# Kernel tuning notes

Measured on AMD Instinct MI355X. Metric: run time of the kernel, lower is better.

Reference implementation:

```python
import jax, jax.numpy as jnp
import numpy as np

N_CLASSES = 10
NBD_PAD = 1
EPS = 1e-5  # nn.LayerNorm default eps


def _neighbor_states(state, n):
    # state: [B, n_classes, H, W]; replicates F.unfold(kernel=2n+1, padding=n)
    # then drops the center tap. Kernel positions enumerated row-major, matching
    # unfold's (C, K2) channel ordering after the view in the torch code.
    B, C, H, W = state.shape
    k = 2 * n + 1
    center = (k * k) // 2
    padded = jnp.pad(state, ((0, 0), (0, 0), (n, n), (n, n)))
    shifts = []
    for idx in range(k * k):
        if idx == center:
            continue
        ki, kj = divmod(idx, k)
        shifts.append(padded[:, :, ki:ki + H, kj:kj + W])
    nb = jnp.stack(shifts, axis=2)  # [B, C, K2-1, H, W]
    return nb.reshape(B, C * (k * k - 1), H, W)


def setup_inputs() -> dict:
    key = jax.random.key(0)
    ks = jax.random.split(key, 7)
    B, C, H, W = 64, 32, 128, 128
    NN_HID, PERC = 128, 112
    x = jax.random.normal(ks[0], (B, C, H, W), dtype=jnp.float32)
    w1 = jax.random.normal(ks[1], (NN_HID, PERC), dtype=jnp.float32) * (1.0 / np.sqrt(PERC))
    b1 = jax.random.normal(ks[2], (NN_HID,), dtype=jnp.float32) * 0.02
    w2 = jax.random.normal(ks[3], (C, NN_HID), dtype=jnp.float32) * (1.0 / np.sqrt(NN_HID))
    b2 = jax.random.normal(ks[4], (C,), dtype=jnp.float32) * 0.02
    gamma = jnp.ones((C,), dtype=jnp.float32) + 0.1 * jax.random.normal(ks[5], (C,), dtype=jnp.float32)
    beta = 0.1 * jax.random.normal(ks[6], (C,), dtype=jnp.float32)
    return {"x": x, "w1": w1, "b1": b1, "w2": w2, "b2": b2, "gamma": gamma, "beta": beta}


def reference(x, w1, b1, w2, b2, gamma, beta):
    # perceive: [B, in_ch + n_classes*(K2-1), H, W]
    nb = _neighbor_states(x[:, :N_CLASSES], NBD_PAD)
    perc = jnp.concatenate([x, nb], axis=1)
    # 1x1 conv MLP (fire_rate == 1.0 -> no update mask)
    h = jax.nn.relu(jnp.einsum('bchw,oc->bohw', perc, w1) + b1[None, :, None, None])
    dx = jnp.einsum('bchw,oc->bohw', h, w2) + b2[None, :, None, None]
    new_state = x + dx
    # clean_slate_if_white: zero hidden channels where argmax class == 0 (no_grad mask)
    pred = jnp.argmax(new_state[:, :N_CLASSES], axis=1)  # [B,H,W]
    inv = jax.lax.stop_gradient((pred != 0).astype(new_state.dtype))[:, None]  # [B,1,H,W]
    new_state = jnp.concatenate(
        [new_state[:, :N_CLASSES], new_state[:, N_CLASSES:] * inv], axis=1)
    # LayerNorm over channel dim (torch permutes to NHWC, norms last dim, permutes back)
    mu = jnp.mean(new_state, axis=1, keepdims=True)
    var = jnp.var(new_state, axis=1, keepdims=True)
    xn = (new_state - mu) * jax.lax.rsqrt(var + EPS)
    return xn * gamma[None, :, None, None] + beta[None, :, None, None]
```

## Files before the change

kernel.cpp:

```cpp
#include <hip/hip_runtime.h>

typedef unsigned short U16;
typedef unsigned int U32;
typedef __bf16 bf16;
typedef bf16 bf16x8 __attribute__((ext_vector_type(8)));
typedef U16  u16x8  __attribute__((ext_vector_type(8)));
typedef float f32x4 __attribute__((ext_vector_type(4)));

__device__ __forceinline__ void split3(float a, U16& o1, U16& o2, U16& o3) {
    U32 ua = __float_as_uint(a);
    float a1 = __uint_as_float(ua & 0xFFFF0000u);
    float r1 = a - a1;
    U32 u2 = __float_as_uint(r1);
    float a2 = __uint_as_float(u2 & 0xFFFF0000u);
    float r2 = r1 - a2;
    o1 = (U16)(ua >> 16);
    o2 = (U16)(u2 >> 16);
    o3 = (U16)(__float_as_uint(r2) >> 16);
}

__device__ __forceinline__ void split3x8(const float v[8], bf16x8& A1, bf16x8& A2, bf16x8& A3) {
    u16x8 e1, e2, e3;
    #pragma unroll
    for (int j = 0; j < 8; ++j) { U16 a, b, c; split3(v[j], a, b, c); e1[j] = a; e2[j] = b; e3[j] = c; }
    A1 = __builtin_bit_cast(bf16x8, e1);
    A2 = __builtin_bit_cast(bf16x8, e2);
    A3 = __builtin_bit_cast(bf16x8, e3);
}

__global__ __launch_bounds__(256)
void prep_kernel(const float* __restrict__ w1g, const float* __restrict__ w2g,
                 U16* __restrict__ w1L, U16* __restrict__ w2L)
{
    int tid = blockIdx.x * 256 + threadIdx.x;
    if (tid < 2048) {
        int n = tid >> 4, k0 = (tid & 15) << 3;
        float v[8];
        #pragma unroll
        for (int j = 0; j < 8; ++j) { int k = k0 + j; v[j] = (k < 112) ? w1g[n * 112 + k] : 0.0f; }
        bf16x8 L1, L2, L3; split3x8(v, L1, L2, L3);
        *(bf16x8*)(w1L + 0 * 16384 + n * 128 + k0) = L1;
        *(bf16x8*)(w1L + 1 * 16384 + n * 128 + k0) = L2;
        *(bf16x8*)(w1L + 2 * 16384 + n * 128 + k0) = L3;
    }
    if (tid < 512) {
        int n = tid >> 4, k0 = (tid & 15) << 3;
        float v[8];
        #pragma unroll
        for (int j = 0; j < 8; ++j) v[j] = w2g[n * 128 + k0 + j];
        bf16x8 L1, L2, L3; split3x8(v, L1, L2, L3);
        *(bf16x8*)(w2L + 0 * 4096 + n * 128 + k0) = L1;
        *(bf16x8*)(w2L + 1 * 4096 + n * 128 + k0) = L2;
        *(bf16x8*)(w2L + 2 * 4096 + n * 128 + k0) = L3;
    }
}

__device__ __forceinline__ void tap_load(const float* __restrict__ xg, int b, int irow,
                                         int jbase, int j, float v[8])
{
    int tpx = j & 63, cls = j >> 6;
    const float* cbase = xg + (b * 32 + cls) * 16384;
    #pragma unroll
    for (int t = 0; t < 8; ++t) {
        int di = (int)((0x22211000u >> (4 * t)) & 0xFu) - 1;
        int dj = (int)((0x21020210u >> (4 * t)) & 0xFu) - 1;
        int row = irow + di;
        int cc  = jbase + tpx + dj;
        bool okb = ((unsigned)row < 128u) && ((unsigned)cc < 128u);
        int off = okb ? (row * 128 + cc) : 0;
        float x = cbase[off];
        v[t] = okb ? x : 0.0f;
    }
}

__device__ __forceinline__ void tap_write(U16* sL, int j, const float v[8])
{
    int tpx = j & 63, cls = j >> 6;
    bf16x8 T1, T2, T3; split3x8(v, T1, T2, T3);
    int to = tpx * 136 + 32 + cls * 8;
    *(bf16x8*)&sL[to] = T1;
    *(bf16x8*)&sL[8704 + to] = T2;
    *(bf16x8*)&sL[17408 + to] = T3;
}

__global__ __launch_bounds__(256, 3)
void cann_kernel(const float* __restrict__ xg,  const U16* __restrict__ w1L,
                 const U16* __restrict__ w2L,
                 const float* __restrict__ b1g, const float* __restrict__ b2g,
                 const float* __restrict__ gg,  const float* __restrict__ bg,
                 float* __restrict__ outg)
{
    __shared__ __align__(16) U16 sL[3 * 8704];

    const int tid  = threadIdx.x;
    const int bid0 = blockIdx.x;
    const int bid  = (bid0 & 7) * 2048 + (bid0 >> 3);
    const int jseg = bid & 1;
    const int irow = (bid >> 1) & 127;
    const int b    = bid >> 8;
    const int jbase = jseg << 6;
    const int lane = tid & 63;
    const int wv   = tid >> 6;
    const int quad = lane >> 4;
    const int col  = lane & 15;

    const int px = tid & 63, cg = tid >> 6;
    const float* srcA = xg + (b * 32 + cg * 8) * 16384 + irow * 128 + jbase + px;
    float va[8];
    #pragma unroll
    for (int i = 0; i < 8; ++i) va[i] = srcA[i * 16384];

    float vt0[8], vt1[8], vt2[8];
    tap_load(xg, b, irow, jbase, tid,       vt0);
    tap_load(xg, b, irow, jbase, tid + 256, vt1);
    if (tid < 128) tap_load(xg, b, irow, jbase, tid + 512, vt2);

    float xs[2][4];
    #pragma unroll
    for (int n2 = 0; n2 < 2; ++n2)
        #pragma unroll
        for (int r = 0; r < 4; ++r)
            xs[n2][r] = xg[(b * 32 + n2 * 16 + col) * 16384 + irow * 128 + jbase
                           + wv * 16 + quad * 4 + r];

    const float b1v0 = b1g[wv * 32 + col];
    const float b1v1 = b1g[wv * 32 + 16 + col];
    const float b2v0 = b2g[col];
    const float b2v1 = b2g[16 + col];
    float g2v[2], be2v[2];
    g2v[0] = gg[col];      g2v[1] = gg[16 + col];
    be2v[0] = bg[col];     be2v[1] = bg[16 + col];

    {
        bf16x8 L1, L2, L3; split3x8(va, L1, L2, L3);
        int o = px * 136 + cg * 8;
        *(bf16x8*)&sL[o] = L1;
        *(bf16x8*)&sL[8704 + o] = L2;
        *(bf16x8*)&sL[17408 + o] = L3;
    }
    tap_write(sL, tid,       vt0);
    tap_write(sL, tid + 256, vt1);
    if (tid < 128) tap_write(sL, tid + 512, vt2);
    if (tid < 128) {
        int zo = (tid >> 1) * 136 + 112 + (tid & 1) * 8;
        uint4 z = make_uint4(0u, 0u, 0u, 0u);
        *(uint4*)&sL[zo] = z;
        *(uint4*)&sL[8704 + zo] = z;
        *(uint4*)&sL[17408 + zo] = z;
    }

    const int n0r = wv * 32 + col;
    bf16x8 bw[2][6];
    #pragma unroll
    for (int L = 0; L < 3; ++L)
        #pragma unroll
        for (int n2 = 0; n2 < 2; ++n2)
            bw[0][L * 2 + n2] =
                *(const bf16x8*)(w1L + L * 16384 + (n0r + n2 * 16) * 128 + quad * 8);

    __syncthreads();

    const f32x4 fz = {0.f, 0.f, 0.f, 0.f};
    f32x4 acc1[4][2];
    #pragma unroll
    for (int mt = 0; mt < 4; ++mt) { acc1[mt][0] = fz; acc1[mt][1] = fz; }

    #pragma unroll
    for (int ks = 0; ks < 4; ++ks) {
        if (ks < 3) {
            #pragma unroll
            for (int L = 0; L < 3; ++L)
                #pragma unroll
                for (int n2 = 0; n2 < 2; ++n2)
                    bw[(ks + 1) & 1][L * 2 + n2] =
                        *(const bf16x8*)(w1L + L * 16384 + (n0r + n2 * 16) * 128
                                         + (ks + 1) * 32 + quad * 8);
        }
        #pragma unroll
        for (int mt = 0; mt < 4; ++mt) {
            int ao = (mt * 16 + col) * 136 + ks * 32 + quad * 8;
            bf16x8 A1 = *(const bf16x8*)&sL[ao];
            bf16x8 A2 = *(const bf16x8*)&sL[8704 + ao];
            bf16x8 A3 = *(const bf16x8*)&sL[17408 + ao];
            #pragma unroll
            for (int n2 = 0; n2 < 2; ++n2) {
                f32x4 a = acc1[mt][n2];
                a = __builtin_amdgcn_mfma_f32_16x16x32_bf16(A1, bw[ks & 1][0 + n2], a, 0, 0, 0);
                a = __builtin_amdgcn_mfma_f32_16x16x32_bf16(A1, bw[ks & 1][2 + n2], a, 0, 0, 0);
                a = __builtin_amdgcn_mfma_f32_16x16x32_bf16(A2, bw[ks & 1][0 + n2], a, 0, 0, 0);
                a = __builtin_amdgcn_mfma_f32_16x16x32_bf16(A1, bw[ks & 1][4 + n2], a, 0, 0, 0);
                a = __builtin_amdgcn_mfma_f32_16x16x32_bf16(A2, bw[ks & 1][2 + n2], a, 0, 0, 0);
                a = __builtin_amdgcn_mfma_f32_16x16x32_bf16(A3, bw[ks & 1][0 + n2], a, 0, 0, 0);
                acc1[mt][n2] = a;
            }
        }
    }
    __syncthreads();

    #pragma unroll
    for (int mt = 0; mt < 4; ++mt)
        #pragma unroll
        for (int n2 = 0; n2 < 2; ++n2) {
            float bb = n2 ? b1v1 : b1v0;
            #pragma unroll
            for (int r = 0; r < 4; ++r) {
                float v = fmaxf(acc1[mt][n2][r] + bb, 0.0f);
                U16 u1, u2, u3; split3(v, u1, u2, u3);
                int ho = (mt * 16 + quad * 4 + r) * 136 + wv * 32 + n2 * 16 + col;
                sL[ho] = u1; sL[8704 + ho] = u2; sL[17408 + ho] = u3;
            }
        }

    bf16x8 w2f[2][6];
    #pragma unroll
    for (int L = 0; L < 3; ++L)
        #pragma unroll
        for (int n2 = 0; n2 < 2; ++n2)
            w2f[0][L * 2 + n2] =
                *(const bf16x8*)(w2L + L * 4096 + (n2 * 16 + col) * 128 + quad * 8);

    __syncthreads();

    f32x4 acc2[2];
    acc2[0] = fz; acc2[1] = fz;
    #pragma unroll
    for (int ks = 0; ks < 4; ++ks) {
        if (ks < 3) {
            #pragma unroll
            for (int L = 0; L < 3; ++L)
                #pragma unroll
                for (int n2 = 0; n2 < 2; ++n2)
                    w2f[(ks + 1) & 1][L * 2 + n2] =
                        *(const bf16x8*)(w2L + L * 4096 + (n2 * 16 + col) * 128
                                         + (ks + 1) * 32 + quad * 8);
        }
        int ho = (wv * 16 + col) * 136 + ks * 32 + quad * 8;
        bf16x8 H1 = *(const bf16x8*)&sL[ho];
        bf16x8 H2 = *(const bf16x8*)&sL[8704 + ho];
        bf16x8 H3 = *(const bf16x8*)&sL[17408 + ho];
        #pragma unroll
        for (int n2 = 0; n2 < 2; ++n2) {
            f32x4 a = acc2[n2];
            a = __builtin_amdgcn_mfma_f32_16x16x32_bf16(H1, w2f[ks & 1][0 + n2], a, 0, 0, 0);
            a = __builtin_amdgcn_mfma_f32_16x16x32_bf16(H1, w2f[ks & 1][2 + n2], a, 0, 0, 0);
            a = __builtin_amdgcn_mfma_f32_16x16x32_bf16(H2, w2f[ks & 1][0 + n2], a, 0, 0, 0);
            a = __builtin_amdgcn_mfma_f32_16x16x32_bf16(H1, w2f[ks & 1][4 + n2], a, 0, 0, 0);
            a = __builtin_amdgcn_mfma_f32_16x16x32_bf16(H2, w2f[ks & 1][2 + n2], a, 0, 0, 0);
            a = __builtin_amdgcn_mfma_f32_16x16x32_bf16(H3, w2f[ks & 1][0 + n2], a, 0, 0, 0);
            acc2[n2] = a;
        }
    }

    float fin[2][4];
    #pragma unroll
    for (int r = 0; r < 4; ++r) {
        float n0 = acc2[0][r] + b2v0 + xs[0][r];
        float n1 = acc2[1][r] + b2v1 + xs[1][r];
        float cm = (col >= 1 && col <= 9) ? n0 : -3.0e38f;
        float z0 = (col == 0)             ? n0 : -3.0e38f;
        #pragma unroll
        for (int m = 1; m < 16; m <<= 1) {
            cm = fmaxf(cm, __shfl_xor(cm, m, 64));
            z0 = fmaxf(z0, __shfl_xor(z0, m, 64));
        }
        float keep = (cm > z0) ? 1.0f : 0.0f;
        n0 = (col >= 10) ? n0 * keep : n0;
        n1 = n1 * keep;
        float s = n0 + n1;
        float q = n0 * n0 + n1 * n1;
        #pragma unroll
        for (int m = 1; m < 16; m <<= 1) {
            s += __shfl_xor(s, m, 64);
            q += __shfl_xor(q, m, 64);
        }
        float mu  = s * 0.03125f;
        float var = q * 0.03125f - mu * mu;
        float rstd = 1.0f / sqrtf(var + 1e-5f);
        fin[0][r] = (n0 - mu) * rstd * g2v[0] + be2v[0];
        fin[1][r] = (n1 - mu) * rstd * g2v[1] + be2v[1];
    }

    __syncthreads();

    float* dxl = (float*)sL;
    #pragma unroll
    for (int n2 = 0; n2 < 2; ++n2)
        #pragma unroll
        for (int r = 0; r < 4; ++r) {
            int p = wv * 16 + quad * 4 + r;
            dxl[p * 37 + n2 * 16 + col] = fin[n2][r];
        }
    __syncthreads();

    {
        int p  = tid & 63;
        int c0 = (tid >> 6) * 8;
        int base = b * 524288 + irow * 128 + jbase + p;
        #pragma unroll
        for (int i = 0; i < 8; ++i)
            outg[base + (c0 + i) * 16384] = dxl[p * 37 + c0 + i];
    }
}

extern "C" void kernel_launch(void* const* d_in, const int* in_sizes, int n_in,
                              void* d_out, int out_size, void* d_ws, size_t ws_size,
                              hipStream_t stream) {
    const float* x  = (const float*)d_in[0];
    const float* w1 = (const float*)d_in[1];
    const float* b1 = (const float*)d_in[2];
    const float* w2 = (const float*)d_in[3];
    const float* b2 = (const float*)d_in[4];
    const float* g  = (const float*)d_in[5];
    const float* be = (const float*)d_in[6];
    float* out = (float*)d_out;

    U16* w1L = (U16*)d_ws;
    U16* w2L = (U16*)((char*)d_ws + 98304);

    hipLaunchKernelGGL(prep_kernel, dim3(8), dim3(256), 0, stream, w1, w2, w1L, w2L);
    hipLaunchKernelGGL(cann_kernel, dim3(16384), dim3(256), 0, stream,
                       x, w1L, w2L, b1, b2, g, be, out);
}
```

Measured before the change: 610.8 us.

## Make fused MLP kernel persistent with next-tile global prefetch

Replaces the launch of one block per 64-pixel tile with a persistent grid of 768 blocks, each looping over 21 or 22 consecutive tiles. While the second GEMM of the current tile runs, the next tile's input and neighbour taps are loaded into registers, so global latency can overlap with MFMA work. __syncthreads is replaced by lighter barrier macros that wait only on LDS counters. The loop keeps a second set of prefetched registers live, which adds register pressure at the declared occupancy, and the original blockIdx swizzle is dropped.

```diff
diff --git a/kernel.cpp b/kernel.cpp
--- a/kernel.cpp
+++ b/kernel.cpp
@@ -54,6 +54,13 @@
         *(bf16x8*)(w2L + 2 * 4096 + n * 128 + k0) = L3;
     }
 }
+
+#define WBAR() do { asm volatile("s_waitcnt lgkmcnt(0)" ::: "memory"); \
+                    __builtin_amdgcn_s_barrier();                      \
+                    asm volatile("" ::: "memory"); } while (0)
+#define RBAR() do { asm volatile("" ::: "memory");                     \
+                    __builtin_amdgcn_s_barrier();                      \
+                    asm volatile("" ::: "memory"); } while (0)
 
 __device__ __forceinline__ void tap_load(const float* __restrict__ xg, int b, int irow,
                                          int jbase, int j, float v[8])
@@ -93,35 +100,13 @@
     __shared__ __align__(16) U16 sL[3 * 8704];
 
     const int tid  = threadIdx.x;
-    const int bid0 = blockIdx.x;
-    const int bid  = (bid0 & 7) * 2048 + (bid0 >> 3);
-    const int jseg = bid & 1;
-    const int irow = (bid >> 1) & 127;
-    const int b    = bid >> 8;
-    const int jbase = jseg << 6;
     const int lane = tid & 63;
     const int wv   = tid >> 6;
     const int quad = lane >> 4;
     const int col  = lane & 15;
-
-    const int px = tid & 63, cg = tid >> 6;
-    const float* srcA = xg + (b * 32 + cg * 8) * 16384 + irow * 128 + jbase + px;
-    float va[8];
-    #pragma unroll
-    for (int i = 0; i < 8; ++i) va[i] = srcA[i * 16384];
-
-    float vt0[8], vt1[8], vt2[8];
-    tap_load(xg, b, irow, jbase, tid,       vt0);
-    tap_load(xg, b, irow, jbase, tid + 256, vt1);
-    if (tid < 128) tap_load(xg, b, irow, jbase, tid + 512, vt2);
-
-    float xs[2][4];
-    #pragma unroll
-    for (int n2 = 0; n2 < 2; ++n2)
-        #pragma unroll
-        for (int r = 0; r < 4; ++r)
-            xs[n2][r] = xg[(b * 32 + n2 * 16 + col) * 16384 + irow * 128 + jbase
-                           + wv * 16 + quad * 4 + r];
+    const int px   = tid & 63;
+    const int cg   = tid >> 6;
+    const int n0r  = wv * 32 + col;
 
     const float b1v0 = b1g[wv * 32 + col];
     const float b1v1 = b1g[wv * 32 + 16 + col];
@@ -131,174 +116,231 @@
     g2v[0] = gg[col];      g2v[1] = gg[16 + col];
     be2v[0] = bg[col];     be2v[1] = bg[16 + col];
 
+    const int bidx = blockIdx.x;
+    int cnt  = (bidx < 256) ? 22 : 21;
+    int tile = (bidx < 256) ? bidx * 22 : bidx * 21 + 256;
+
+    int b = tile >> 8, irow = (tile >> 1) & 127, jbase = (tile & 1) << 6;
+
+    float va[8], vt0[8], vt1[8], vt2[8], xs[2][4];
     {
-        bf16x8 L1, L2, L3; split3x8(va, L1, L2, L3);
-        int o = px * 136 + cg * 8;
-        *(bf16x8*)&sL[o] = L1;
-        *(bf16x8*)&sL[8704 + o] = L2;
-        *(bf16x8*)&sL[17408 + o] = L3;
-    }
-    tap_write(sL, tid,       vt0);
-    tap_write(sL, tid + 256, vt1);
-    if (tid < 128) tap_write(sL, tid + 512, vt2);
-    if (tid < 128) {
-        int zo = (tid >> 1) * 136 + 112 + (tid & 1) * 8;
-        uint4 z = make_uint4(0u, 0u, 0u, 0u);
-        *(uint4*)&sL[zo] = z;
-        *(uint4*)&sL[8704 + zo] = z;
-        *(uint4*)&sL[17408 + zo] = z;
-    }
-
-    const int n0r = wv * 32 + col;
-    bf16x8 bw[2][6];
-    #pragma unroll
-    for (int L = 0; L < 3; ++L)
+        const float* srcA = xg + (b * 32 + cg * 8) * 16384 + irow * 128 + jbase + px;
+        #pragma unroll
+        for (int i = 0; i < 8; ++i) va[i] = srcA[i * 16384];
+        tap_load(xg, b, irow, jbase, tid,       vt0);
+        tap_load(xg, b, irow, jbase, tid + 256, vt1);
+        if (tid < 128) tap_load(xg, b, irow, jbase, tid + 512, vt2);
         #pragma unroll
         for (int n2 = 0; n2 < 2; ++n2)
-            bw[0][L * 2 + n2] =
-                *(const bf16x8*)(w1L + L * 16384 + (n0r + n2 * 16) * 128 + quad * 8);
-
-    __syncthreads();
+            #pragma unroll
+            for (int r = 0; r < 4; ++r)
+                xs[n2][r] = xg[(b * 32 + n2 * 16 + col) * 16384 + irow * 128 + jbase
+                               + wv * 16 + quad * 4 + r];
+    }
 
     const f32x4 fz = {0.f, 0.f, 0.f, 0.f};
-    f32x4 acc1[4][2];
-    #pragma unroll
-    for (int mt = 0; mt < 4; ++mt) { acc1[mt][0] = fz; acc1[mt][1] = fz; }
-
-    #pragma unroll
-    for (int ks = 0; ks < 4; ++ks) {
-        if (ks < 3) {
-            #pragma unroll
-            for (int L = 0; L < 3; ++L)
-                #pragma unroll
-                for (int n2 = 0; n2 < 2; ++n2)
-                    bw[(ks + 1) & 1][L * 2 + n2] =
-                        *(const bf16x8*)(w1L + L * 16384 + (n0r + n2 * 16) * 128
-                                         + (ks + 1) * 32 + quad * 8);
-        }
-        #pragma unroll
-        for (int mt = 0; mt < 4; ++mt) {
-            int ao = (mt * 16 + col) * 136 + ks * 32 + quad * 8;
-            bf16x8 A1 = *(const bf16x8*)&sL[ao];
-            bf16x8 A2 = *(const bf16x8*)&sL[8704 + ao];
-            bf16x8 A3 = *(const bf16x8*)&sL[17408 + ao];
+
+    #pragma unroll 1
+    for (int it = 0; ; ++it) {
+        {
+            bf16x8 L1, L2, L3; split3x8(va, L1, L2, L3);
+            int o = px * 136 + cg * 8;
+            *(bf16x8*)&sL[o] = L1;
+            *(bf16x8*)&sL[8704 + o] = L2;
+            *(bf16x8*)&sL[17408 + o] = L3;
+        }
+        tap_write(sL, tid,       vt0);
+        tap_write(sL, tid + 256, vt1);
+        if (tid < 128) tap_write(sL, tid + 512, vt2);
+        if (tid < 128) {
+            int zo = (tid >> 1) * 136 + 112 + (tid & 1) * 8;
+            uint4 z = make_uint4(0u, 0u, 0u, 0u);
+            *(uint4*)&sL[zo] = z;
+            *(uint4*)&sL[8704 + zo] = z;
+            *(uint4*)&sL[17408 + zo] = z;
+        }
+
+        bf16x8 bw[2][6];
+        #pragma unroll
+        for (int L = 0; L < 3; ++L)
+            #pragma unroll
+            for (int n2 = 0; n2 < 2; ++n2)
+                bw[0][L * 2 + n2] =
+                    *(const bf16x8*)(w1L + L * 16384 + (n0r + n2 * 16) * 128 + quad * 8);
+
+        WBAR();
+
+        f32x4 acc1[4][2];
+        #pragma unroll
+        for (int mt = 0; mt < 4; ++mt) { acc1[mt][0] = fz; acc1[mt][1] = fz; }
+
+        #pragma unroll
+        for (int ks = 0; ks < 4; ++ks) {
+            if (ks < 3) {
+                #pragma unroll
+                for (int L = 0; L < 3; ++L)
+                    #pragma unroll
+                    for (int n2 = 0; n2 < 2; ++n2)
+                        bw[(ks + 1) & 1][L * 2 + n2] =
+                            *(const bf16x8*)(w1L + L * 16384 + (n0r + n2 * 16) * 128
+                                             + (ks + 1) * 32 + quad * 8);
+            }
+            #pragma unroll
+            for (int mt = 0; mt < 4; ++mt) {
+                int ao = (mt * 16 + col) * 136 + ks * 32 + quad * 8;
+                bf16x8 A1 = *(const bf16x8*)&sL[ao];
+                bf16x8 A2 = *(const bf16x8*)&sL[8704 + ao];
+                bf16x8 A3 = *(const bf16x8*)&sL[17408 + ao];
+                #pragma unroll
+                for (int n2 = 0; n2 < 2; ++n2) {
+                    f32x4 a = acc1[mt][n2];
+                    a = __builtin_amdgcn_mfma_f32_16x16x32_bf16(A1, bw[ks & 1][0 + n2], a, 0, 0, 0);
+                    a = __builtin_amdgcn_mfma_f32_16x16x32_bf16(A1, bw[ks & 1][2 + n2], a, 0, 0, 0);
+                    a = __builtin_amdgcn_mfma_f32_16x16x32_bf16(A2, bw[ks & 1][0 + n2], a, 0, 0, 0);
+                    a = __builtin_amdgcn_mfma_f32_16x16x32_bf16(A1, bw[ks & 1][4 + n2], a, 0, 0, 0);
+                    a = __builtin_amdgcn_mfma_f32_16x16x32_bf16(A2, bw[ks & 1][2 + n2], a, 0, 0, 0);
+                    a = __builtin_amdgcn_mfma_f32_16x16x32_bf16(A3, bw[ks & 1][0 + n2], a, 0, 0, 0);
+                    acc1[mt][n2] = a;
+                }
+            }
+        }
+
+        RBAR();
+
+        #pragma unroll
+        for (int mt = 0; mt < 4; ++mt)
             #pragma unroll
             for (int n2 = 0; n2 < 2; ++n2) {
-                f32x4 a = acc1[mt][n2];
-                a = __builtin_amdgcn_mfma_f32_16x16x32_bf16(A1, bw[ks & 1][0 + n2], a, 0, 0, 0);
-                a = __builtin_amdgcn_mfma_f32_16x16x32_bf16(A1, bw[ks & 1][2 + n2], a, 0, 0, 0);
-                a = __builtin_amdgcn_mfma_f32_16x16x32_bf16(A2, bw[ks & 1][0 + n2], a, 0, 0, 0);
-                a = __builtin_amdgcn_mfma_f32_16x16x32_bf16(A1, bw[ks & 1][4 + n2], a, 0, 0, 0);
-                a = __builtin_amdgcn_mfma_f32_16x16x32_bf16(A2, bw[ks & 1][2 + n2], a, 0, 0, 0);
-                a = __builtin_amdgcn_mfma_f32_16x16x32_bf16(A3, bw[ks & 1][0 + n2], a, 0, 0, 0);
-                acc1[mt][n2] = a;
-            }
-        }
-    }
-    __syncthreads();
-
-    #pragma unroll
-    for (int mt = 0; mt < 4; ++mt)
-        #pragma unroll
-        for (int n2 = 0; n2 < 2; ++n2) {
-            float bb = n2 ? b1v1 : b1v0;
+                float bb = n2 ? b1v1 : b1v0;
+                #pragma unroll
+                for (int r = 0; r < 4; ++r) {
+                    float v = fmaxf(acc1[mt][n2][r] + bb, 0.0f);
+                    U16 u1, u2, u3; split3(v, u1, u2, u3);
+                    int ho = (mt * 16 + quad * 4 + r) * 136 + wv * 32 + n2 * 16 + col;
+                    sL[ho] = u1; sL[8704 + ho] = u2; sL[17408 + ho] = u3;
+                }
+            }
+
+        bf16x8 w2f[2][6];
+        #pragma unroll
+        for (int L = 0; L < 3; ++L)
+            #pragma unroll
+            for (int n2 = 0; n2 < 2; ++n2)
+                w2f[0][L * 2 + n2] =
+                    *(const bf16x8*)(w2L + L * 4096 + (n2 * 16 + col) * 128 + quad * 8);
+
+        const bool more = (it + 1 < cnt);
+        int nb = b, nirow = irow, njbase = jbase;
+        float xsn[2][4];
+        if (more) {
+            int nt = tile + 1;
+            nb = nt >> 8; nirow = (nt >> 1) & 127; njbase = (nt & 1) << 6;
+            const float* srcA = xg + (nb * 32 + cg * 8) * 16384 + nirow * 128 + njbase + px;
+            #pragma unroll
+            for (int i = 0; i < 8; ++i) va[i] = srcA[i * 16384];
+            tap_load(xg, nb, nirow, njbase, tid,       vt0);
+            tap_load(xg, nb, nirow, njbase, tid + 256, vt1);
+            if (tid < 128) tap_load(xg, nb, nirow, njbase, tid + 512, vt2);
+            #pragma unroll
+            for (int n2 = 0; n2 < 2; ++n2)
+                #pragma unroll
+                for (int r = 0; r < 4; ++r)
+                    xsn[n2][r] = xg[(nb * 32 + n2 * 16 + col) * 16384 + nirow * 128 + njbase
+                                    + wv * 16 + quad * 4 + r];
+        }
+
+        WBAR();
+
+        f32x4 acc2[2];
+        acc2[0] = fz; acc2[1] = fz;
+        #pragma unroll
+        for (int ks = 0; ks < 4; ++ks) {
+            if (ks < 3) {
+                #pragma unroll
+                for (int L = 0; L < 3; ++L)
+                    #pragma unroll
+                    for (int n2 = 0; n2 < 2; ++n2)
+                        w2f[(ks + 1) & 1][L * 2 + n2] =
+                            *(const bf16x8*)(w2L + L * 4096 + (n2 * 16 + col) * 128
+                                             + (ks + 1) * 32 + quad * 8);
+            }
+            int ho = (wv * 16 + col) * 136 + ks * 32 + quad * 8;
+            bf16x8 H1 = *(const bf16x8*)&sL[ho];
+            bf16x8 H2 = *(const bf16x8*)&sL[8704 + ho];
+            bf16x8 H3 = *(const bf16x8*)&sL[17408 + ho];
+            #pragma unroll
+            for (int n2 = 0; n2 < 2; ++n2) {
+                f32x4 a = acc2[n2];
+                a = __builtin_amdgcn_mfma_f32_16x16x32_bf16(H1, w2f[ks & 1][0 + n2], a, 0, 0, 0);
+                a = __builtin_amdgcn_mfma_f32_16x16x32_bf16(H1, w2f[ks & 1][2 + n2], a, 0, 0, 0);
+                a = __builtin_amdgcn_mfma_f32_16x16x32_bf16(H2, w2f[ks & 1][0 + n2], a, 0, 0, 0);
+                a = __builtin_amdgcn_mfma_f32_16x16x32_bf16(H1, w2f[ks & 1][4 + n2], a, 0, 0, 0);
+                a = __builtin_amdgcn_mfma_f32_16x16x32_bf16(H2, w2f[ks & 1][2 + n2], a, 0, 0, 0);
+                a = __builtin_amdgcn_mfma_f32_16x16x32_bf16(H3, w2f[ks & 1][0 + n2], a, 0, 0, 0);
+                acc2[n2] = a;
+            }
+        }
+
+        float fin[2][4];
+        #pragma unroll
+        for (int r = 0; r < 4; ++r) {
+            float n0 = acc2[0][r] + b2v0 + xs[0][r];
+            float n1 = acc2[1][r] + b2v1 + xs[1][r];
+            float cm = (col >= 1 && col <= 9) ? n0 : -3.0e38f;
+            float z0 = (col == 0)             ? n0 : -3.0e38f;
+            #pragma unroll
+            for (int m = 1; m < 16; m <<= 1) {
+                cm = fmaxf(cm, __shfl_xor(cm, m, 64));
+                z0 = fmaxf(z0, __shfl_xor(z0, m, 64));
+            }
+            float keep = (cm > z0) ? 1.0f : 0.0f;
+            n0 = (col >= 10) ? n0 * keep : n0;
+            n1 = n1 * keep;
+            float s = n0 + n1;
+            float q = n0 * n0 + n1 * n1;
+            #pragma unroll
+            for (int m = 1; m < 16; m <<= 1) {
+                s += __shfl_xor(s, m, 64);
+                q += __shfl_xor(q, m, 64);
+            }
+            float mu  = s * 0.03125f;
+            float var = q * 0.03125f - mu * mu;
+            float rstd = 1.0f / sqrtf(var + 1e-5f);
+            fin[0][r] = (n0 - mu) * rstd * g2v[0] + be2v[0];
+            fin[1][r] = (n1 - mu) * rstd * g2v[1] + be2v[1];
+        }
+
+        RBAR();
+
+        float* dxl = (float*)sL;
+        #pragma unroll
+        for (int n2 = 0; n2 < 2; ++n2)
             #pragma unroll
             for (int r = 0; r < 4; ++r) {
-                float v = fmaxf(acc1[mt][n2][r] + bb, 0.0f);
-                U16 u1, u2, u3; split3(v, u1, u2, u3);
-                int ho = (mt * 16 + quad * 4 + r) * 136 + wv * 32 + n2 * 16 + col;
-                sL[ho] = u1; sL[8704 + ho] = u2; sL[17408 + ho] = u3;
-            }
-        }
-
-    bf16x8 w2f[2][6];
-    #pragma unroll
-    for (int L = 0; L < 3; ++L)
+                int p = wv * 16 + quad * 4 + r;
+                dxl[p * 37 + n2 * 16 + col] = fin[n2][r];
+            }
+
+        WBAR();
+
+        {
+            int p  = tid & 63;
+            int c0 = (tid >> 6) * 8;
+            int base = b * 524288 + irow * 128 + jbase + p;
+            #pragma unroll
+            for (int i = 0; i < 8; ++i)
+                outg[base + (c0 + i) * 16384] = dxl[p * 37 + c0 + i];
+        }
+
+        if (!more) break;
+
+        RBAR();
+
+        tile += 1; b = nb; irow = nirow; jbase = njbase;
         #pragma unroll
         for (int n2 = 0; n2 < 2; ++n2)
-            w2f[0][L * 2 + n2] =
-                *(const bf16x8*)(w2L + L * 4096 + (n2 * 16 + col) * 128 + quad * 8);
-
-    __syncthreads();
-
-    f32x4 acc2[2];
-    acc2[0] = fz; acc2[1] = fz;
-    #pragma unroll
-    for (int ks = 0; ks < 4; ++ks) {
-        if (ks < 3) {
-            #pragma unroll
-            for (int L = 0; L < 3; ++L)
-                #pragma unroll
-                for (int n2 = 0; n2 < 2; ++n2)
-                    w2f[(ks + 1) & 1][L * 2 + n2] =
-                        *(const bf16x8*)(w2L + L * 4096 + (n2 * 16 + col) * 128
-                                         + (ks + 1) * 32 + quad * 8);
-        }
-        int ho = (wv * 16 + col) * 136 + ks * 32 + quad * 8;
-        bf16x8 H1 = *(const bf16x8*)&sL[ho];
-        bf16x8 H2 = *(const bf16x8*)&sL[8704 + ho];
-        bf16x8 H3 = *(const bf16x8*)&sL[17408 + ho];
-        #pragma unroll
-        for (int n2 = 0; n2 < 2; ++n2) {
-            f32x4 a = acc2[n2];
-            a = __builtin_amdgcn_mfma_f32_16x16x32_bf16(H1, w2f[ks & 1][0 + n2], a, 0, 0, 0);
-            a = __builtin_amdgcn_mfma_f32_16x16x32_bf16(H1, w2f[ks & 1][2 + n2], a, 0, 0, 0);
-            a = __builtin_amdgcn_mfma_f32_16x16x32_bf16(H2, w2f[ks & 1][0 + n2], a, 0, 0, 0);
-            a = __builtin_amdgcn_mfma_f32_16x16x32_bf16(H1, w2f[ks & 1][4 + n2], a, 0, 0, 0);
-            a = __builtin_amdgcn_mfma_f32_16x16x32_bf16(H2, w2f[ks & 1][2 + n2], a, 0, 0, 0);
-            a = __builtin_amdgcn_mfma_f32_16x16x32_bf16(H3, w2f[ks & 1][0 + n2], a, 0, 0, 0);
-            acc2[n2] = a;
-        }
-    }
-
-    float fin[2][4];
-    #pragma unroll
-    for (int r = 0; r < 4; ++r) {
-        float n0 = acc2[0][r] + b2v0 + xs[0][r];
-        float n1 = acc2[1][r] + b2v1 + xs[1][r];
-        float cm = (col >= 1 && col <= 9) ? n0 : -3.0e38f;
-        float z0 = (col == 0)             ? n0 : -3.0e38f;
-        #pragma unroll
-        for (int m = 1; m < 16; m <<= 1) {
-            cm = fmaxf(cm, __shfl_xor(cm, m, 64));
-            z0 = fmaxf(z0, __shfl_xor(z0, m, 64));
-        }
-        float keep = (cm > z0) ? 1.0f : 0.0f;
-        n0 = (col >= 10) ? n0 * keep : n0;
-        n1 = n1 * keep;
-        float s = n0 + n1;
-        float q = n0 * n0 + n1 * n1;
-        #pragma unroll
-        for (int m = 1; m < 16; m <<= 1) {
-            s += __shfl_xor(s, m, 64);
-            q += __shfl_xor(q, m, 64);
-        }
-        float mu  = s * 0.03125f;
-        float var = q * 0.03125f - mu * mu;
-        float rstd = 1.0f / sqrtf(var + 1e-5f);
-        fin[0][r] = (n0 - mu) * rstd * g2v[0] + be2v[0];
-        fin[1][r] = (n1 - mu) * rstd * g2v[1] + be2v[1];
-    }
-
-    __syncthreads();
-
-    float* dxl = (float*)sL;
-    #pragma unroll
-    for (int n2 = 0; n2 < 2; ++n2)
-        #pragma unroll
-        for (int r = 0; r < 4; ++r) {
-            int p = wv * 16 + quad * 4 + r;
-            dxl[p * 37 + n2 * 16 + col] = fin[n2][r];
-        }
-    __syncthreads();
-
-    {
-        int p  = tid & 63;
-        int c0 = (tid >> 6) * 8;
-        int base = b * 524288 + irow * 128 + jbase + p;
-        #pragma unroll
-        for (int i = 0; i < 8; ++i)
-            outg[base + (c0 + i) * 16384] = dxl[p * 37 + c0 + i];
+            #pragma unroll
+            for (int r = 0; r < 4; ++r) xs[n2][r] = xsn[n2][r];
     }
 }
 
@@ -318,6 +360,6 @@
     U16* w2L = (U16*)((char*)d_ws + 98304);
 
     hipLaunchKernelGGL(prep_kernel, dim3(8), dim3(256), 0, stream, w1, w2, w1L, w2L);
-    hipLaunchKernelGGL(cann_kernel, dim3(16384), dim3(256), 0, stream,
+    hipLaunchKernelGGL(cann_kernel, dim3(768), dim3(256), 0, stream,
                        x, w1L, w2L, b1, b2, g, be, out);
 }
```

Result: slower. 849.7 us (+39.1%).

## Give each wave its own pixel rows across all hidden units to drop barriers

Applied to the files above, without the earlier changes.

The layer-1 work split changes from each wave owning 32 hidden units for all 64 pixels to each wave owning 16 pixels for all 128 hidden units. Each wave then reads and writes only its own rows of shared memory, so the barriers between layer 1, layer 2 and the store epilogue can be removed; the epilogue transpose also uses a per-wave shared region. The cost is that every wave now loads all of w1 straight from global or cache inside the loop, without the earlier register double-buffer, which is roughly four times more weight-load traffic per block. The block-index swizzle is also removed.

```diff
diff --git a/kernel.cpp b/kernel.cpp
--- a/kernel.cpp
+++ b/kernel.cpp
@@ -93,8 +93,7 @@
     __shared__ __align__(16) U16 sL[3 * 8704];
 
     const int tid  = threadIdx.x;
-    const int bid0 = blockIdx.x;
-    const int bid  = (bid0 & 7) * 2048 + (bid0 >> 3);
+    const int bid  = blockIdx.x;
     const int jseg = bid & 1;
     const int irow = (bid >> 1) & 127;
     const int b    = bid >> 8;
@@ -103,8 +102,9 @@
     const int wv   = tid >> 6;
     const int quad = lane >> 4;
     const int col  = lane & 15;
-
-    const int px = tid & 63, cg = tid >> 6;
+    const int px   = tid & 63;
+    const int cg   = tid >> 6;
+
     const float* srcA = xg + (b * 32 + cg * 8) * 16384 + irow * 128 + jbase + px;
     float va[8];
     #pragma unroll
@@ -123,8 +123,9 @@
             xs[n2][r] = xg[(b * 32 + n2 * 16 + col) * 16384 + irow * 128 + jbase
                            + wv * 16 + quad * 4 + r];
 
-    const float b1v0 = b1g[wv * 32 + col];
-    const float b1v1 = b1g[wv * 32 + 16 + col];
+    float b1f[8];
+    #pragma unroll
+    for (int nt = 0; nt < 8; ++nt) b1f[nt] = b1g[nt * 16 + col];
     const float b2v0 = b2g[col];
     const float b2v1 = b2g[16 + col];
     float g2v[2], be2v[2];
@@ -149,104 +150,85 @@
         *(uint4*)&sL[17408 + zo] = z;
     }
 
-    const int n0r = wv * 32 + col;
-    bf16x8 bw[2][6];
-    #pragma unroll
-    for (int L = 0; L < 3; ++L)
-        #pragma unroll
-        for (int n2 = 0; n2 < 2; ++n2)
-            bw[0][L * 2 + n2] =
-                *(const bf16x8*)(w1L + L * 16384 + (n0r + n2 * 16) * 128 + quad * 8);
-
-    __syncthreads();
+    bf16x8 pw0, pw1, pw2;
+    {
+        const U16* wp = w1L + col * 128 + quad * 8;
+        pw0 = *(const bf16x8*)(wp);
+        pw1 = *(const bf16x8*)(wp + 16384);
+        pw2 = *(const bf16x8*)(wp + 32768);
+    }
+
+    asm volatile("s_waitcnt lgkmcnt(0)" ::: "memory");
+    __builtin_amdgcn_s_barrier();
+    asm volatile("" ::: "memory");
 
     const f32x4 fz = {0.f, 0.f, 0.f, 0.f};
-    f32x4 acc1[4][2];
-    #pragma unroll
-    for (int mt = 0; mt < 4; ++mt) { acc1[mt][0] = fz; acc1[mt][1] = fz; }
+    f32x4 acc1[8];
+    #pragma unroll
+    for (int nt = 0; nt < 8; ++nt) acc1[nt] = fz;
 
     #pragma unroll
     for (int ks = 0; ks < 4; ++ks) {
-        if (ks < 3) {
-            #pragma unroll
-            for (int L = 0; L < 3; ++L)
-                #pragma unroll
-                for (int n2 = 0; n2 < 2; ++n2)
-                    bw[(ks + 1) & 1][L * 2 + n2] =
-                        *(const bf16x8*)(w1L + L * 16384 + (n0r + n2 * 16) * 128
-                                         + (ks + 1) * 32 + quad * 8);
-        }
-        #pragma unroll
-        for (int mt = 0; mt < 4; ++mt) {
-            int ao = (mt * 16 + col) * 136 + ks * 32 + quad * 8;
-            bf16x8 A1 = *(const bf16x8*)&sL[ao];
-            bf16x8 A2 = *(const bf16x8*)&sL[8704 + ao];
-            bf16x8 A3 = *(const bf16x8*)&sL[17408 + ao];
-            #pragma unroll
-            for (int n2 = 0; n2 < 2; ++n2) {
-                f32x4 a = acc1[mt][n2];
-                a = __builtin_amdgcn_mfma_f32_16x16x32_bf16(A1, bw[ks & 1][0 + n2], a, 0, 0, 0);
-                a = __builtin_amdgcn_mfma_f32_16x16x32_bf16(A1, bw[ks & 1][2 + n2], a, 0, 0, 0);
-                a = __builtin_amdgcn_mfma_f32_16x16x32_bf16(A2, bw[ks & 1][0 + n2], a, 0, 0, 0);
-                a = __builtin_amdgcn_mfma_f32_16x16x32_bf16(A1, bw[ks & 1][4 + n2], a, 0, 0, 0);
-                a = __builtin_amdgcn_mfma_f32_16x16x32_bf16(A2, bw[ks & 1][2 + n2], a, 0, 0, 0);
-                a = __builtin_amdgcn_mfma_f32_16x16x32_bf16(A3, bw[ks & 1][0 + n2], a, 0, 0, 0);
-                acc1[mt][n2] = a;
+        const int ao = (wv * 16 + col) * 136 + ks * 32 + quad * 8;
+        bf16x8 A1 = *(const bf16x8*)&sL[ao];
+        bf16x8 A2 = *(const bf16x8*)&sL[8704 + ao];
+        bf16x8 A3 = *(const bf16x8*)&sL[17408 + ao];
+        #pragma unroll
+        for (int nt = 0; nt < 8; ++nt) {
+            bf16x8 B1, B2, B3;
+            if (ks == 0 && nt == 0) { B1 = pw0; B2 = pw1; B3 = pw2; }
+            else {
+                const U16* wp = w1L + (nt * 16 + col) * 128 + ks * 32 + quad * 8;
+                B1 = *(const bf16x8*)(wp);
+                B2 = *(const bf16x8*)(wp + 16384);
+                B3 = *(const bf16x8*)(wp + 32768);
             }
-        }
-    }
-    __syncthreads();
-
-    #pragma unroll
-    for (int mt = 0; mt < 4; ++mt)
-        #pragma unroll
-        for (int n2 = 0; n2 < 2; ++n2) {
-            float bb = n2 ? b1v1 : b1v0;
-            #pragma unroll
-            for (int r = 0; r < 4; ++r) {
-                float v = fmaxf(acc1[mt][n2][r] + bb, 0.0f);
-                U16 u1, u2, u3; split3(v, u1, u2, u3);
-                int ho = (mt * 16 + quad * 4 + r) * 136 + wv * 32 + n2 * 16 + col;
-                sL[ho] = u1; sL[8704 + ho] = u2; sL[17408 + ho] = u3;
-            }
-        }
-
-    bf16x8 w2f[2][6];
-    #pragma unroll
-    for (int L = 0; L < 3; ++L)
-        #pragma unroll
-        for (int n2 = 0; n2 < 2; ++n2)
-            w2f[0][L * 2 + n2] =
-                *(const bf16x8*)(w2L + L * 4096 + (n2 * 16 + col) * 128 + quad * 8);
-
-    __syncthreads();
+            f32x4 a = acc1[nt];
+            a = __builtin_amdgcn_mfma_f32_16x16x32_bf16(A1, B1, a, 0, 0, 0);
+            a = __builtin_amdgcn_mfma_f32_16x16x32_bf16(A1, B2, a, 0, 0, 0);
+            a = __builtin_amdgcn_mfma_f32_16x16x32_bf16(A2, B1, a, 0, 0, 0);
+            a = __builtin_amdgcn_mfma_f32_16x16x32_bf16(A1, B3, a, 0, 0, 0);
+            a = __builtin_amdgcn_mfma_f32_16x16x32_bf16(A2, B2, a, 0, 0, 0);
+            a = __builtin_amdgcn_mfma_f32_16x16x32_bf16(A3, B1, a, 0, 0, 0);
+            acc1[nt] = a;
+        }
+    }
+
+    #pragma unroll
+    for (int nt = 0; nt < 8; ++nt) {
+        float bb = b1f[nt];
+        #pragma unroll
+        for (int r = 0; r < 4; ++r) {
+            float v = fmaxf(acc1[nt][r] + bb, 0.0f);
+            U16 u1, u2, u3; split3(v, u1, u2, u3);
+            int ho = (wv * 16 + quad * 4 + r) * 136 + nt * 16 + col;
+            sL[ho] = u1; sL[8704 + ho] = u2; sL[17408 + ho] = u3;
+        }
+    }
+    asm volatile("" ::: "memory");
 
     f32x4 acc2[2];
     acc2[0] = fz; acc2[1] = fz;
     #pragma unroll
     for (int ks = 0; ks < 4; ++ks) {
-        if (ks < 3) {
-            #pragma unroll
-            for (int L = 0; L < 3; ++L)
-                #pragma unroll
-                for (int n2 = 0; n2 < 2; ++n2)
-                    w2f[(ks + 1) & 1][L * 2 + n2] =
-                        *(const bf16x8*)(w2L + L * 4096 + (n2 * 16 + col) * 128
-                                         + (ks + 1) * 32 + quad * 8);
-        }
-        int ho = (wv * 16 + col) * 136 + ks * 32 + quad * 8;
+        int k0 = ks * 32 + quad * 8;
+        int ho = (wv * 16 + col) * 136 + k0;
         bf16x8 H1 = *(const bf16x8*)&sL[ho];
         bf16x8 H2 = *(const bf16x8*)&sL[8704 + ho];
         bf16x8 H3 = *(const bf16x8*)&sL[17408 + ho];
         #pragma unroll
         for (int n2 = 0; n2 < 2; ++n2) {
+            const U16* wp = w2L + (n2 * 16 + col) * 128 + k0;
+            bf16x8 B1 = *(const bf16x8*)(wp);
+            bf16x8 B2 = *(const bf16x8*)(wp + 4096);
+            bf16x8 B3 = *(const bf16x8*)(wp + 8192);
             f32x4 a = acc2[n2];
-            a = __builtin_amdgcn_mfma_f32_16x16x32_bf16(H1, w2f[ks & 1][0 + n2], a, 0, 0, 0);
-            a = __builtin_amdgcn_mfma_f32_16x16x32_bf16(H1, w2f[ks & 1][2 + n2], a, 0, 0, 0);
-            a = __builtin_amdgcn_mfma_f32_16x16x32_bf16(H2, w2f[ks & 1][0 + n2], a, 0, 0, 0);
-            a = __builtin_amdgcn_mfma_f32_16x16x32_bf16(H1, w2f[ks & 1][4 + n2], a, 0, 0, 0);
-            a = __builtin_amdgcn_mfma_f32_16x16x32_bf16(H2, w2f[ks & 1][2 + n2], a, 0, 0, 0);
-            a = __builtin_amdgcn_mfma_f32_16x16x32_bf16(H3, w2f[ks & 1][0 + n2], a, 0, 0, 0);
+            a = __builtin_amdgcn_mfma_f32_16x16x32_bf16(H1, B1, a, 0, 0, 0);
+            a = __builtin_amdgcn_mfma_f32_16x16x32_bf16(H1, B2, a, 0, 0, 0);
+            a = __builtin_amdgcn_mfma_f32_16x16x32_bf16(H2, B1, a, 0, 0, 0);
+            a = __builtin_amdgcn_mfma_f32_16x16x32_bf16(H1, B3, a, 0, 0, 0);
+            a = __builtin_amdgcn_mfma_f32_16x16x32_bf16(H2, B2, a, 0, 0, 0);
+            a = __builtin_amdgcn_mfma_f32_16x16x32_bf16(H3, B1, a, 0, 0, 0);
             acc2[n2] = a;
         }
     }
@@ -280,25 +262,26 @@
         fin[1][r] = (n1 - mu) * rstd * g2v[1] + be2v[1];
     }
 
-    __syncthreads();
-
-    float* dxl = (float*)sL;
+    asm volatile("" ::: "memory");
+    float* dxs = (float*)(sL + wv * 2176);
     #pragma unroll
     for (int n2 = 0; n2 < 2; ++n2)
         #pragma unroll
         for (int r = 0; r < 4; ++r) {
-            int p = wv * 16 + quad * 4 + r;
-            dxl[p * 37 + n2 * 16 + col] = fin[n2][r];
-        }
-    __syncthreads();
+            int p = quad * 4 + r;
+            dxs[p * 33 + n2 * 16 + col] = fin[n2][r];
+        }
+    asm volatile("" ::: "memory");
 
     {
-        int p  = tid & 63;
-        int c0 = (tid >> 6) * 8;
-        int base = b * 524288 + irow * 128 + jbase + p;
-        #pragma unroll
-        for (int i = 0; i < 8; ++i)
-            outg[base + (c0 + i) * 16384] = dxl[p * 37 + c0 + i];
+        int cq   = lane >> 4;
+        int pcol = lane & 15;
+        int base = b * 524288 + irow * 128 + jbase + wv * 16 + pcol;
+        #pragma unroll
+        for (int i = 0; i < 8; ++i) {
+            int ch = i * 4 + cq;
+            outg[base + ch * 16384] = dxs[pcol * 33 + ch];
+        }
     }
 }
 
```

New measurement: 1.093 ms. 1.79x slower.
